# Kernel optimization log

Measured on AMD Instinct MI355X. Metric: run time of the kernel, lower is better.

## Reference

```python
import jax, jax.numpy as jnp
import numpy as np

DIM = 768
H = 64
W = 64
NB = 8
BS = DIM // NB
LAMBD = 0.01
SCALE = 0.02


def softshrink(x, lambd):
    return jnp.sign(x) * jnp.maximum(jnp.abs(x) - lambd, 0.0)


def setup_inputs() -> dict:
    key = jax.random.key(0)
    ks = jax.random.split(key, 7)
    x = jax.random.normal(ks[0], (8, H * W, DIM), dtype=jnp.float32)
    w1 = SCALE * jax.random.normal(ks[1], (2, NB, BS, BS), dtype=jnp.float32)
    b1 = SCALE * jax.random.normal(ks[2], (2, NB, BS), dtype=jnp.float32)
    w2 = SCALE * jax.random.normal(ks[3], (2, NB, BS, BS), dtype=jnp.float32)
    b2 = SCALE * jax.random.normal(ks[4], (2, NB, BS), dtype=jnp.float32)
    # Conv1d(dim, dim, kernel_size=1) == per-token linear: weight [C_out, C_in], bias [C_out]
    Wb = (1.0 / np.sqrt(DIM)) * jax.random.normal(ks[5], (DIM, DIM), dtype=jnp.float32)
    bb = (1.0 / np.sqrt(DIM)) * jax.random.normal(ks[6], (DIM,), dtype=jnp.float32)
    return {"x": x, "w1": w1, "b1": b1, "w2": w2, "b2": b2, "Wb": Wb, "bb": bb}


def reference(x, w1, b1, w2, b2, Wb, bb):
    B, N, C = x.shape
    # bias path: Conv1d with kernel 1 is a linear map over channels
    bias = jnp.einsum('bnc,dc->bnd', x, Wb) + bb
    # spectral path
    xg = x.reshape(B, H, W, C)
    xf = jnp.fft.rfft2(xg, axes=(1, 2), norm='ortho')          # [B, H, W//2+1, C] complex64
    xf = xf.reshape(B, H, W // 2 + 1, NB, BS)
    xr, xi = jnp.real(xf), jnp.imag(xf)
    # layer 1: complex block-diagonal matmul + relu
    r1 = jax.nn.relu(jnp.einsum('...bd,bdk->...bk', xr, w1[0])
                     - jnp.einsum('...bd,bdk->...bk', xi, w1[1]) + b1[0])
    i1 = jax.nn.relu(jnp.einsum('...bd,bdk->...bk', xr, w1[1])
                     + jnp.einsum('...bd,bdk->...bk', xi, w1[0]) + b1[1])
    # layer 2
    r2 = (jnp.einsum('...bd,bdk->...bk', r1, w2[0])
          - jnp.einsum('...bd,bdk->...bk', i1, w2[1]) + b2[0])
    i2 = (jnp.einsum('...bd,bdk->...bk', r1, w2[1])
          + jnp.einsum('...bd,bdk->...bk', i1, w2[0]) + b2[1])
    r2 = softshrink(r2, LAMBD)
    i2 = softshrink(i2, LAMBD)
    xc = (r2 + 1j * i2).reshape(B, H, W // 2 + 1, C)
    xo = jnp.fft.irfft2(xc, s=(H, W), axes=(1, 2), norm='ortho')  # [B, H, W, C]
    return xo.reshape(B, N, C) + bias
```

## Files before the change

### kernel.cpp

```cpp
#include <hip/hip_runtime.h>
#include <math.h>

#ifndef M_PI
#define M_PI 3.14159265358979323846
#endif

namespace {

constexpr int kDim = 768;
constexpr int kNKW = 33;
constexpr int kB = 8;
constexpr float kLambd = 0.01f;
constexpr size_t kXFElems = (size_t)kB * kNKW * 64 * kDim;

typedef __attribute__((ext_vector_type(8))) __bf16 bf16x8;
typedef __attribute__((ext_vector_type(8))) short short8;
typedef __attribute__((ext_vector_type(4))) float f32x4;

alignas(16) __device__ unsigned short g_wT[4 * 8 * 96 * 96];

__device__ inline unsigned short f2bf(float f) {
  unsigned int u = __float_as_uint(f);
  unsigned int r = (u + 0x7FFFu + ((u >> 16) & 1u)) >> 16;
  return (unsigned short)r;
}

__device__ inline bf16x8 s2b(short8 s) { return __builtin_bit_cast(bf16x8, s); }
__device__ inline bf16x8 negb(short8 s) {
  s ^= (short)0x8000;
  return __builtin_bit_cast(bf16x8, s);
}

__device__ inline void gload_lds16(const void* g, void* l) {
  __builtin_amdgcn_global_load_lds(
      (const __attribute__((address_space(1))) unsigned int*)g,
      (__attribute__((address_space(3))) unsigned int*)l, 16, 0, 0);
}

__global__ __launch_bounds__(256) void cvt_f32_bf16_kernel(
    const float* __restrict__ in, unsigned short* __restrict__ out, int n4) {
  int i = blockIdx.x * 256 + threadIdx.x;
  if (i >= n4) return;
  const float4 v = reinterpret_cast<const float4*>(in)[i];
  ushort4 o;
  o.x = f2bf(v.x); o.y = f2bf(v.y); o.z = f2bf(v.z); o.w = f2bf(v.w);
  reinterpret_cast<ushort4*>(out)[i] = o;
}

__global__ __launch_bounds__(256) void cvt_w_kernel(
    const float* __restrict__ w1, const float* __restrict__ w2) {
  const int e = blockIdx.x * 256 + threadIdx.x;
  if (e >= 4 * 8 * 96 * 96) return;
  const int k = e % 96;
  const int d = (e / 96) % 96;
  const int nbm = e / 9216;
  const int mtx = nbm >> 3;
  const int nb = nbm & 7;
  const float* src =
      (mtx < 2 ? w1 : w2) + ((size_t)(mtx & 1) * 8 + nb) * 9216;
  g_wT[((size_t)nbm * 96 + k) * 96 + d] = f2bf(src[d * 96 + k]);
}

__global__ __launch_bounds__(256) void mfma_gemm_kernel(
    const unsigned short* __restrict__ xbf, const unsigned short* __restrict__ wbf,
    const float* __restrict__ bb, float* __restrict__ out) {
  __shared__ unsigned short As[128 * 32];
  __shared__ unsigned short Bs[128 * 32];
  const int t = threadIdx.x;
  const int lane = t & 63;
  const int wid = t >> 6;
  const int wm = wid >> 1;
  const int wn = wid & 1;
  const int id = blockIdx.x;
  const int swz = (id & 7) * 192 + (id >> 3);
  const int m0 = (swz / 6) * 128;
  const int n0 = (swz % 6) * 128;

  f32x4 acc[4][4];
#pragma unroll
  for (int i = 0; i < 4; ++i)
#pragma unroll
    for (int j = 0; j < 4; ++j) acc[i][j] = (f32x4){0.f, 0.f, 0.f, 0.f};

  char* AsB = (char*)As;
  char* BsB = (char*)Bs;
  const int cl = lane & 15;
  const int kg = lane >> 4;

  for (int k0 = 0; k0 < 768; k0 += 32) {
#pragma unroll
    for (int i = 0; i < 2; ++i) {
      const int off = (wid * 2 + i) * 1024 + lane * 16;
      const int row = off >> 6;
      const int kb = off & 63;
      const char* gA = (const char*)xbf + ((size_t)(m0 + row) * 768 + k0) * 2 + kb;
      gload_lds16(gA, AsB + (wid * 2 + i) * 1024);
      const char* gB = (const char*)wbf + ((size_t)(n0 + row) * 768 + k0) * 2 + kb;
      gload_lds16(gB, BsB + (wid * 2 + i) * 1024);
    }
    asm volatile("s_waitcnt vmcnt(0)" ::: "memory");
    __syncthreads();

    bf16x8 av[4], bv[4];
#pragma unroll
    for (int mi = 0; mi < 4; ++mi) {
      const int r = wm * 64 + mi * 16 + cl;
      av[mi] = *reinterpret_cast<const bf16x8*>(AsB + r * 64 + kg * 16);
    }
#pragma unroll
    for (int ni = 0; ni < 4; ++ni) {
      const int r = wn * 64 + ni * 16 + cl;
      bv[ni] = *reinterpret_cast<const bf16x8*>(BsB + r * 64 + kg * 16);
    }
#pragma unroll
    for (int mi = 0; mi < 4; ++mi)
#pragma unroll
      for (int ni = 0; ni < 4; ++ni)
        acc[mi][ni] = __builtin_amdgcn_mfma_f32_16x16x32_bf16(
            av[mi], bv[ni], acc[mi][ni], 0, 0, 0);
    __syncthreads();
  }

#pragma unroll
  for (int ni = 0; ni < 4; ++ni) {
    const int n = n0 + wn * 64 + ni * 16 + cl;
    const float bias = bb[n];
#pragma unroll
    for (int mi = 0; mi < 4; ++mi) {
      const int m = m0 + wm * 64 + mi * 16 + kg * 4;
#pragma unroll
      for (int r = 0; r < 4; ++r) {
        out[(size_t)(m + r) * 768 + n] = acc[mi][ni][r] + bias;
      }
    }
  }
}

__global__ __launch_bounds__(256) void rfft_row_mfma_kernel(
    const float* __restrict__ x, unsigned short* __restrict__ xbf,
    unsigned short* __restrict__ XFr, unsigned short* __restrict__ XFi) {
  __shared__ alignas(16) unsigned short Cs[48 * 80];
  __shared__ alignas(16) unsigned short Ss[48 * 80];
  __shared__ alignas(16) unsigned short xs[64 * 66];
  const int t = threadIdx.x;
  for (int e = t; e < 48 * 64; e += 256) {
    const int kh = e >> 6;
    const int w = e & 63;
    const float ang = (float)(2.0 * M_PI / 64.0) * (float)((kh * w) & 63);
    float s_, c_;
    __sincosf(ang, &s_, &c_);
    Cs[kh * 80 + w] = f2bf(0.125f * c_);
    Ss[kh * 80 + w] = f2bf(-0.125f * s_);
  }

  const int lane = t & 63;
  const int wv = t >> 6;
  const int cl = lane & 15;
  const int kg = lane >> 4;
  const int bh = blockIdx.x;
  const int b = bh >> 6;
  const int h = bh & 63;
  const int c0 = blockIdx.y * 64;

  {
    const float* xrow = x + (size_t)bh * (64 * 768) + c0;
    unsigned short* xbrow = xbf + (size_t)bh * (64 * 768) + c0;
#pragma unroll 4
    for (int it = 0; it < 16; ++it) {
      const int w = wv * 16 + it;
      const float v = xrow[(size_t)w * 768 + lane];
      const unsigned short bv = f2bf(v);
      xbrow[(size_t)w * 768 + lane] = bv;
      xs[w * 66 + lane] = bv;
    }
  }
  __syncthreads();

  const int cA = wv * 16 + cl;
  short8 ax[2];
#pragma unroll
  for (int kf = 0; kf < 2; ++kf) {
#pragma unroll
    for (int j = 0; j < 8; ++j)
      ax[kf][j] = (short)xs[(kf * 32 + kg * 8 + j) * 66 + cA];
  }

  f32x4 aR[3], aI[3];
#pragma unroll
  for (int nt = 0; nt < 3; ++nt) {
    aR[nt] = (f32x4){0.f, 0.f, 0.f, 0.f};
    aI[nt] = (f32x4){0.f, 0.f, 0.f, 0.f};
  }

#pragma unroll
  for (int nt = 0; nt < 3; ++nt) {
#pragma unroll
    for (int kf = 0; kf < 2; ++kf) {
      const int row = nt * 16 + cl;
      const int w0 = kf * 32 + kg * 8;
      const bf16x8 bc = *reinterpret_cast<const bf16x8*>(Cs + row * 80 + w0);
      const bf16x8 bs = *reinterpret_cast<const bf16x8*>(Ss + row * 80 + w0);
      aR[nt] = __builtin_amdgcn_mfma_f32_16x16x32_bf16(s2b(ax[kf]), bc, aR[nt], 0, 0, 0);
      aI[nt] = __builtin_amdgcn_mfma_f32_16x16x32_bf16(s2b(ax[kf]), bs, aI[nt], 0, 0, 0);
    }
  }

  const int cD = c0 + wv * 16 + kg * 4;
#pragma unroll
  for (int nt = 0; nt < 3; ++nt) {
    const int kh = nt * 16 + cl;
    if (kh <= 32) {
      const size_t off = (((size_t)b * kNKW + kh) * 64 + h) * 768 + cD;
      ushort4 vr, vi;
      vr.x = f2bf(aR[nt][0]); vr.y = f2bf(aR[nt][1]);
      vr.z = f2bf(aR[nt][2]); vr.w = f2bf(aR[nt][3]);
      vi.x = f2bf(aI[nt][0]); vi.y = f2bf(aI[nt][1]);
      vi.z = f2bf(aI[nt][2]); vi.w = f2bf(aI[nt][3]);
      *reinterpret_cast<ushort4*>(XFr + off) = vr;
      *reinterpret_cast<ushort4*>(XFi + off) = vi;
    }
  }
}

template <int SIGN>
__global__ __launch_bounds__(256) void fft_col_mfma_kernel(
    unsigned short* __restrict__ Xr, unsigned short* __restrict__ Xi) {
  __shared__ alignas(16) unsigned short Cs[64 * 80];
  __shared__ alignas(16) unsigned short Ss[64 * 80];
  const int t = threadIdx.x;
  for (int e = t; e < 4096; e += 256) {
    const int kh = e >> 6;
    const int h = e & 63;
    const float ang = (float)(2.0 * M_PI / 64.0) * (float)((kh * h) & 63);
    float s_, c_;
    __sincosf(ang, &s_, &c_);
    Cs[kh * 80 + h] = f2bf(0.125f * c_);
    Ss[kh * 80 + h] = f2bf(0.125f * (float)SIGN * s_);
  }
  __syncthreads();

  const int lane = t & 63;
  const int wv = t >> 6;
  const int cl = lane & 15;
  const int kg = lane >> 4;
  const size_t cbase =
      (size_t)blockIdx.x * (64 * 768) + blockIdx.y * 64 + wv * 16 + cl;

  f32x4 aR[4], aI[4];
#pragma unroll
  for (int mi = 0; mi < 4; ++mi) {
    aR[mi] = (f32x4){0.f, 0.f, 0.f, 0.f};
    aI[mi] = (f32x4){0.f, 0.f, 0.f, 0.f};
  }

#pragma unroll
  for (int kf = 0; kf < 2; ++kf) {
    const int h0 = kf * 32 + kg * 8;
    short8 brf, bif;
#pragma unroll
    for (int j = 0; j < 8; ++j) {
      brf[j] = (short)Xr[cbase + (size_t)(h0 + j) * 768];
      bif[j] = (short)Xi[cbase + (size_t)(h0 + j) * 768];
    }
    const bf16x8 bxr = s2b(brf);
    const bf16x8 bxi = s2b(bif);
    const bf16x8 bxin = negb(bif);
#pragma unroll
    for (int mi = 0; mi < 4; ++mi) {
      const int arow = mi * 16 + cl;
      const bf16x8 ac =
          *reinterpret_cast<const bf16x8*>(Cs + arow * 80 + h0);
      const bf16x8 as =
          *reinterpret_cast<const bf16x8*>(Ss + arow * 80 + h0);
      aR[mi] = __builtin_amdgcn_mfma_f32_16x16x32_bf16(ac, bxr, aR[mi], 0, 0, 0);
      aR[mi] = __builtin_amdgcn_mfma_f32_16x16x32_bf16(as, bxin, aR[mi], 0, 0, 0);
      aI[mi] = __builtin_amdgcn_mfma_f32_16x16x32_bf16(ac, bxi, aI[mi], 0, 0, 0);
      aI[mi] = __builtin_amdgcn_mfma_f32_16x16x32_bf16(as, bxr, aI[mi], 0, 0, 0);
    }
  }

#pragma unroll
  for (int mi = 0; mi < 4; ++mi) {
#pragma unroll
    for (int r = 0; r < 4; ++r) {
      const int kh = mi * 16 + kg * 4 + r;
      Xr[cbase + (size_t)kh * 768] = f2bf(aR[mi][r]);
      Xi[cbase + (size_t)kh * 768] = f2bf(aI[mi][r]);
    }
  }
}

__global__ __launch_bounds__(512) void mlp_mfma_kernel(
    unsigned short* __restrict__ Xr, unsigned short* __restrict__ Xi,
    const float* __restrict__ b1, const float* __restrict__ b2) {
  __shared__ unsigned short sXr[128 * 104];
  __shared__ unsigned short sXi[128 * 104];
  const int t = threadIdx.x;
  const int lane = t & 63;
  const int wid = t >> 6;
  const int wm = wid >> 1;
  const int wn = wid & 1;
  const int cl = lane & 15;
  const int kg = lane >> 4;
  const int nb = blockIdx.y;
  const size_t p0 = (size_t)blockIdx.x * 128;

  {
    const int row = t >> 2;
    const int q = t & 3;
    const size_t gbase = (p0 + row) * 768 + nb * 96 + q * 24;
    unsigned short* lr = sXr + row * 104 + q * 24;
    unsigned short* li = sXi + row * 104 + q * 24;
#pragma unroll
    for (int v = 0; v < 3; ++v) {
      *reinterpret_cast<short8*>(lr + v * 8) =
          *reinterpret_cast<const short8*>(Xr + gbase + v * 8);
      *reinterpret_cast<short8*>(li + v * 8) =
          *reinterpret_cast<const short8*>(Xi + gbase + v * 8);
    }
  }
  __syncthreads();

  const unsigned short* wt1r = g_wT + (size_t)(0 * 8 + nb) * 9216;
  const unsigned short* wt1i = g_wT + (size_t)(1 * 8 + nb) * 9216;
  const unsigned short* wt2r = g_wT + (size_t)(2 * 8 + nb) * 9216;
  const unsigned short* wt2i = g_wT + (size_t)(3 * 8 + nb) * 9216;

  f32x4 aR[2][3], aI[2][3];
#pragma unroll
  for (int mf = 0; mf < 2; ++mf)
#pragma unroll
    for (int nf = 0; nf < 3; ++nf) {
      aR[mf][nf] = (f32x4){0.f, 0.f, 0.f, 0.f};
      aI[mf][nf] = (f32x4){0.f, 0.f, 0.f, 0.f};
    }

#pragma unroll
  for (int kk = 0; kk < 3; ++kk) {
    const int ko = kk * 32 + kg * 8;
    short8 xr_[2], xi_[2];
#pragma unroll
    for (int mf = 0; mf < 2; ++mf) {
      const int r = wm * 32 + mf * 16 + cl;
      xr_[mf] = *reinterpret_cast<const short8*>(sXr + r * 104 + ko);
      xi_[mf] = *reinterpret_cast<const short8*>(sXi + r * 104 + ko);
    }
    short8 wr_[3], wi_[3];
#pragma unroll
    for (int nf = 0; nf < 3; ++nf) {
      const int r = wn * 48 + nf * 16 + cl;
      wr_[nf] = *reinterpret_cast<const short8*>(wt1r + r * 96 + ko);
      wi_[nf] = *reinterpret_cast<const short8*>(wt1i + r * 96 + ko);
    }
#pragma unroll
    for (int mf = 0; mf < 2; ++mf) {
      const bf16x8 axr = s2b(xr_[mf]);
      const bf16x8 axi = s2b(xi_[mf]);
      const bf16x8 axin = negb(xi_[mf]);
#pragma unroll
      for (int nf = 0; nf < 3; ++nf) {
        aR[mf][nf] = __builtin_amdgcn_mfma_f32_16x16x32_bf16(axr, s2b(wr_[nf]), aR[mf][nf], 0, 0, 0);
        aR[mf][nf] = __builtin_amdgcn_mfma_f32_16x16x32_bf16(axin, s2b(wi_[nf]), aR[mf][nf], 0, 0, 0);
        aI[mf][nf] = __builtin_amdgcn_mfma_f32_16x16x32_bf16(axr, s2b(wi_[nf]), aI[mf][nf], 0, 0, 0);
        aI[mf][nf] = __builtin_amdgcn_mfma_f32_16x16x32_bf16(axi, s2b(wr_[nf]), aI[mf][nf], 0, 0, 0);
      }
    }
  }
  __syncthreads();

#pragma unroll
  for (int nf = 0; nf < 3; ++nf) {
    const int col = wn * 48 + nf * 16 + cl;
    const float br = b1[nb * 96 + col];
    const float bi = b1[768 + nb * 96 + col];
#pragma unroll
    for (int mf = 0; mf < 2; ++mf) {
#pragma unroll
      for (int r = 0; r < 4; ++r) {
        const int m = wm * 32 + mf * 16 + kg * 4 + r;
        const float vr = fmaxf(aR[mf][nf][r] + br, 0.f);
        const float vi = fmaxf(aI[mf][nf][r] + bi, 0.f);
        sXr[m * 104 + col] = f2bf(vr);
        sXi[m * 104 + col] = f2bf(vi);
      }
    }
  }
  __syncthreads();

#pragma unroll
  for (int mf = 0; mf < 2; ++mf)
#pragma unroll
    for (int nf = 0; nf < 3; ++nf) {
      aR[mf][nf] = (f32x4){0.f, 0.f, 0.f, 0.f};
      aI[mf][nf] = (f32x4){0.f, 0.f, 0.f, 0.f};
    }
#pragma unroll
  for (int kk = 0; kk < 3; ++kk) {
    const int ko = kk * 32 + kg * 8;
    short8 xr_[2], xi_[2];
#pragma unroll
    for (int mf = 0; mf < 2; ++mf) {
      const int r = wm * 32 + mf * 16 + cl;
      xr_[mf] = *reinterpret_cast<const short8*>(sXr + r * 104 + ko);
      xi_[mf] = *reinterpret_cast<const short8*>(sXi + r * 104 + ko);
    }
    short8 wr_[3], wi_[3];
#pragma unroll
    for (int nf = 0; nf < 3; ++nf) {
      const int r = wn * 48 + nf * 16 + cl;
      wr_[nf] = *reinterpret_cast<const short8*>(wt2r + r * 96 + ko);
      wi_[nf] = *reinterpret_cast<const short8*>(wt2i + r * 96 + ko);
    }
#pragma unroll
    for (int mf = 0; mf < 2; ++mf) {
      const bf16x8 axr = s2b(xr_[mf]);
      const bf16x8 axi = s2b(xi_[mf]);
      const bf16x8 axin = negb(xi_[mf]);
#pragma unroll
      for (int nf = 0; nf < 3; ++nf) {
        aR[mf][nf] = __builtin_amdgcn_mfma_f32_16x16x32_bf16(axr, s2b(wr_[nf]), aR[mf][nf], 0, 0, 0);
        aR[mf][nf] = __builtin_amdgcn_mfma_f32_16x16x32_bf16(axin, s2b(wi_[nf]), aR[mf][nf], 0, 0, 0);
        aI[mf][nf] = __builtin_amdgcn_mfma_f32_16x16x32_bf16(axr, s2b(wi_[nf]), aI[mf][nf], 0, 0, 0);
        aI[mf][nf] = __builtin_amdgcn_mfma_f32_16x16x32_bf16(axi, s2b(wr_[nf]), aI[mf][nf], 0, 0, 0);
      }
    }
  }

#pragma unroll
  for (int nf = 0; nf < 3; ++nf) {
    const int col = wn * 48 + nf * 16 + cl;
    const float br = b2[nb * 96 + col];
    const float bi = b2[768 + nb * 96 + col];
    const int gc = nb * 96 + col;
#pragma unroll
    for (int mf = 0; mf < 2; ++mf) {
#pragma unroll
      for (int r = 0; r < 4; ++r) {
        const int m = wm * 32 + mf * 16 + kg * 4 + r;
        float vr = aR[mf][nf][r] + br;
        float vi = aI[mf][nf][r] + bi;
        vr = (vr > kLambd) ? (vr - kLambd) : ((vr < -kLambd) ? (vr + kLambd) : 0.f);
        vi = (vi > kLambd) ? (vi - kLambd) : ((vi < -kLambd) ? (vi + kLambd) : 0.f);
        Xr[(p0 + m) * 768 + gc] = f2bf(vr);
        Xi[(p0 + m) * 768 + gc] = f2bf(vi);
      }
    }
  }
}

__global__ __launch_bounds__(256) void irfft_row_add_mfma_kernel(
    const unsigned short* __restrict__ Zr, const unsigned short* __restrict__ Zi,
    float* __restrict__ out) {
  __shared__ alignas(16) unsigned short Ac[64 * 80];
  __shared__ alignas(16) unsigned short Asn[64 * 80];
  const int t = threadIdx.x;
  for (int e = t; e < 4096; e += 256) {
    const int w = e >> 6;
    const int kw = e & 63;
    unsigned short cv = 0, sv = 0;
    if (kw < 33) {
      const float a = (kw == 0 || kw == 32) ? 0.125f : 0.25f;
      const float ang = (float)(2.0 * M_PI / 64.0) * (float)((kw * w) & 63);
      float s_, c_;
      __sincosf(ang, &s_, &c_);
      cv = f2bf(a * c_);
      sv = f2bf(-a * s_);
    }
    Ac[w * 80 + kw] = cv;
    Asn[w * 80 + kw] = sv;
  }
  __syncthreads();

  const int lane = t & 63;
  const int wv = t >> 6;
  const int cl = lane & 15;
  const int kg = lane >> 4;
  const int bh = blockIdx.x;
  const int b = bh >> 6;
  const int h = bh & 63;
  const int cb = blockIdx.y * 64 + wv * 16;

  const int cA = cb + cl;
  short8 azr[2], azi[2];
#pragma unroll
  for (int kf = 0; kf < 2; ++kf) {
#pragma unroll
    for (int j = 0; j < 8; ++j) {
      const int kw = kf * 32 + kg * 8 + j;
      short zr = 0, zi = 0;
      if (kw < 33) {
        const size_t off = (((size_t)b * kNKW + kw) * 64 + h) * 768 + cA;
        zr = (short)Zr[off];
        zi = (short)Zi[off];
      }
      azr[kf][j] = zr;
      azi[kf][j] = zi;
    }
  }

  const int cD = cb + kg * 4;
  float* obase = out + ((size_t)bh * 64) * 768;
  f32x4 aO[4];
#pragma unroll
  for (int nt = 0; nt < 4; ++nt) {
    const int w = nt * 16 + cl;
    aO[nt] = *reinterpret_cast<const f32x4*>(obase + (size_t)w * 768 + cD);
  }

#pragma unroll
  for (int nt = 0; nt < 4; ++nt) {
#pragma unroll
    for (int kf = 0; kf < 2; ++kf) {
      const int row = nt * 16 + cl;
      const int kw0 = kf * 32 + kg * 8;
      const bf16x8 bc = *reinterpret_cast<const bf16x8*>(Ac + row * 80 + kw0);
      const bf16x8 bs = *reinterpret_cast<const bf16x8*>(Asn + row * 80 + kw0);
      aO[nt] = __builtin_amdgcn_mfma_f32_16x16x32_bf16(s2b(azr[kf]), bc, aO[nt], 0, 0, 0);
      aO[nt] = __builtin_amdgcn_mfma_f32_16x16x32_bf16(s2b(azi[kf]), bs, aO[nt], 0, 0, 0);
    }
  }

#pragma unroll
  for (int nt = 0; nt < 4; ++nt) {
    const int w = nt * 16 + cl;
    *reinterpret_cast<f32x4*>(obase + (size_t)w * 768 + cD) = aO[nt];
  }
}

}

extern "C" void kernel_launch(void* const* d_in, const int* in_sizes, int n_in,
                              void* d_out, int out_size, void* d_ws,
                              size_t ws_size, hipStream_t stream) {
  (void)in_sizes; (void)n_in; (void)out_size;
  const float* x  = (const float*)d_in[0];
  const float* w1 = (const float*)d_in[1];
  const float* b1 = (const float*)d_in[2];
  const float* w2 = (const float*)d_in[3];
  const float* b2 = (const float*)d_in[4];
  const float* Wb = (const float*)d_in[5];
  const float* bb = (const float*)d_in[6];
  float* out = (float*)d_out;

  if (ws_size < 2 * kXFElems * sizeof(float)) return;
  unsigned short* xbf = (unsigned short*)d_ws;
  unsigned short* wbf = xbf + (size_t)32768 * 768;
  unsigned short* XFr = wbf + (size_t)768 * 768;
  unsigned short* XFi = XFr + kXFElems;

  cvt_f32_bf16_kernel<<<dim3((768 * 768 / 4 + 255) / 256), 256, 0, stream>>>(
      Wb, wbf, 768 * 768 / 4);
  cvt_w_kernel<<<dim3(4 * 8 * 96 * 96 / 256), 256, 0, stream>>>(w1, w2);
  rfft_row_mfma_kernel<<<dim3(512, 12), 256, 0, stream>>>(x, xbf, XFr, XFi);
  mfma_gemm_kernel<<<dim3(1536), 256, 0, stream>>>(xbf, wbf, bb, out);
  fft_col_mfma_kernel<-1><<<dim3(264, 12), 256, 0, stream>>>(XFr, XFi);
  mlp_mfma_kernel<<<dim3(132, 8), 512, 0, stream>>>(XFr, XFi, b1, b2);
  fft_col_mfma_kernel<1><<<dim3(264, 12), 256, 0, stream>>>(XFr, XFi);
  irfft_row_add_mfma_kernel<<<dim3(512, 12), 256, 0, stream>>>(XFr, XFi, out);
}
```

Before: 252.6 us.

## Fuse column FFT, spectral MLP, and inverse column FFT into one kernel

Replaces the forward column DFT, block-diagonal complex MLP and inverse column DFT kernels with a single kernel. Each block loads one 64-row by 96-channel slab into LDS and runs all three stages there, writing back once. This removes two full round-trips of the spectral buffers through global memory and two kernel launches. Twiddle tables are now computed once by a small init kernel into global memory and read directly, instead of being rebuilt with sincos in every block. The cost is a 256-thread MLP tile with more LDS per block, strided LDS gathers for the DFT operands, and twiddle reads that go through global memory and cache.

```diff
diff --git a/kernel.cpp b/kernel.cpp
--- a/kernel.cpp
+++ b/kernel.cpp
@@ -18,6 +18,10 @@
 typedef __attribute__((ext_vector_type(4))) float f32x4;
 
 alignas(16) __device__ unsigned short g_wT[4 * 8 * 96 * 96];
+alignas(16) __device__ unsigned short g_twC[64 * 64];
+alignas(16) __device__ unsigned short g_twS[64 * 64];
+alignas(16) __device__ unsigned short g_iwC[64 * 64];
+alignas(16) __device__ unsigned short g_iwS[64 * 64];
 
 __device__ inline unsigned short f2bf(float f) {
   unsigned int u = __float_as_uint(f);
@@ -35,6 +39,26 @@
   __builtin_amdgcn_global_load_lds(
       (const __attribute__((address_space(1))) unsigned int*)g,
       (__attribute__((address_space(3))) unsigned int*)l, 16, 0, 0);
+}
+
+__global__ __launch_bounds__(256) void init_tables_kernel() {
+  const int e = blockIdx.x * 256 + threadIdx.x;
+  if (e >= 4096) return;
+  const int a = e >> 6;
+  const int bcol = e & 63;
+  const float ang = (float)(2.0 * M_PI / 64.0) * (float)((a * bcol) & 63);
+  float s_, c_;
+  __sincosf(ang, &s_, &c_);
+  g_twC[e] = f2bf(0.125f * c_);
+  g_twS[e] = f2bf(0.125f * s_);
+  unsigned short cv = 0, sv = 0;
+  if (bcol < 33) {
+    const float al = (bcol == 0 || bcol == 32) ? 0.125f : 0.25f;
+    cv = f2bf(al * c_);
+    sv = f2bf(-al * s_);
+  }
+  g_iwC[e] = cv;
+  g_iwS[e] = sv;
 }
 
 __global__ __launch_bounds__(256) void cvt_f32_bf16_kernel(
@@ -139,20 +163,8 @@
 __global__ __launch_bounds__(256) void rfft_row_mfma_kernel(
     const float* __restrict__ x, unsigned short* __restrict__ xbf,
     unsigned short* __restrict__ XFr, unsigned short* __restrict__ XFi) {
-  __shared__ alignas(16) unsigned short Cs[48 * 80];
-  __shared__ alignas(16) unsigned short Ss[48 * 80];
   __shared__ alignas(16) unsigned short xs[64 * 66];
   const int t = threadIdx.x;
-  for (int e = t; e < 48 * 64; e += 256) {
-    const int kh = e >> 6;
-    const int w = e & 63;
-    const float ang = (float)(2.0 * M_PI / 64.0) * (float)((kh * w) & 63);
-    float s_, c_;
-    __sincosf(ang, &s_, &c_);
-    Cs[kh * 80 + w] = f2bf(0.125f * c_);
-    Ss[kh * 80 + w] = f2bf(-0.125f * s_);
-  }
-
   const int lane = t & 63;
   const int wv = t >> 6;
   const int cl = lane & 15;
@@ -198,10 +210,10 @@
     for (int kf = 0; kf < 2; ++kf) {
       const int row = nt * 16 + cl;
       const int w0 = kf * 32 + kg * 8;
-      const bf16x8 bc = *reinterpret_cast<const bf16x8*>(Cs + row * 80 + w0);
-      const bf16x8 bs = *reinterpret_cast<const bf16x8*>(Ss + row * 80 + w0);
-      aR[nt] = __builtin_amdgcn_mfma_f32_16x16x32_bf16(s2b(ax[kf]), bc, aR[nt], 0, 0, 0);
-      aI[nt] = __builtin_amdgcn_mfma_f32_16x16x32_bf16(s2b(ax[kf]), bs, aI[nt], 0, 0, 0);
+      const short8 cs = *reinterpret_cast<const short8*>(g_twC + row * 64 + w0);
+      const short8 ss = *reinterpret_cast<const short8*>(g_twS + row * 64 + w0);
+      aR[nt] = __builtin_amdgcn_mfma_f32_16x16x32_bf16(s2b(ax[kf]), s2b(cs), aR[nt], 0, 0, 0);
+      aI[nt] = __builtin_amdgcn_mfma_f32_16x16x32_bf16(s2b(ax[kf]), negb(ss), aI[nt], 0, 0, 0);
     }
   }
 
@@ -222,79 +234,13 @@
   }
 }
 
-template <int SIGN>
-__global__ __launch_bounds__(256) void fft_col_mfma_kernel(
-    unsigned short* __restrict__ Xr, unsigned short* __restrict__ Xi) {
-  __shared__ alignas(16) unsigned short Cs[64 * 80];
-  __shared__ alignas(16) unsigned short Ss[64 * 80];
-  const int t = threadIdx.x;
-  for (int e = t; e < 4096; e += 256) {
-    const int kh = e >> 6;
-    const int h = e & 63;
-    const float ang = (float)(2.0 * M_PI / 64.0) * (float)((kh * h) & 63);
-    float s_, c_;
-    __sincosf(ang, &s_, &c_);
-    Cs[kh * 80 + h] = f2bf(0.125f * c_);
-    Ss[kh * 80 + h] = f2bf(0.125f * (float)SIGN * s_);
-  }
-  __syncthreads();
-
-  const int lane = t & 63;
-  const int wv = t >> 6;
-  const int cl = lane & 15;
-  const int kg = lane >> 4;
-  const size_t cbase =
-      (size_t)blockIdx.x * (64 * 768) + blockIdx.y * 64 + wv * 16 + cl;
-
-  f32x4 aR[4], aI[4];
-#pragma unroll
-  for (int mi = 0; mi < 4; ++mi) {
-    aR[mi] = (f32x4){0.f, 0.f, 0.f, 0.f};
-    aI[mi] = (f32x4){0.f, 0.f, 0.f, 0.f};
-  }
-
-#pragma unroll
-  for (int kf = 0; kf < 2; ++kf) {
-    const int h0 = kf * 32 + kg * 8;
-    short8 brf, bif;
-#pragma unroll
-    for (int j = 0; j < 8; ++j) {
-      brf[j] = (short)Xr[cbase + (size_t)(h0 + j) * 768];
-      bif[j] = (short)Xi[cbase + (size_t)(h0 + j) * 768];
-    }
-    const bf16x8 bxr = s2b(brf);
-    const bf16x8 bxi = s2b(bif);
-    const bf16x8 bxin = negb(bif);
-#pragma unroll
-    for (int mi = 0; mi < 4; ++mi) {
-      const int arow = mi * 16 + cl;
-      const bf16x8 ac =
-          *reinterpret_cast<const bf16x8*>(Cs + arow * 80 + h0);
-      const bf16x8 as =
-          *reinterpret_cast<const bf16x8*>(Ss + arow * 80 + h0);
-      aR[mi] = __builtin_amdgcn_mfma_f32_16x16x32_bf16(ac, bxr, aR[mi], 0, 0, 0);
-      aR[mi] = __builtin_amdgcn_mfma_f32_16x16x32_bf16(as, bxin, aR[mi], 0, 0, 0);
-      aI[mi] = __builtin_amdgcn_mfma_f32_16x16x32_bf16(ac, bxi, aI[mi], 0, 0, 0);
-      aI[mi] = __builtin_amdgcn_mfma_f32_16x16x32_bf16(as, bxr, aI[mi], 0, 0, 0);
-    }
-  }
-
-#pragma unroll
-  for (int mi = 0; mi < 4; ++mi) {
-#pragma unroll
-    for (int r = 0; r < 4; ++r) {
-      const int kh = mi * 16 + kg * 4 + r;
-      Xr[cbase + (size_t)kh * 768] = f2bf(aR[mi][r]);
-      Xi[cbase + (size_t)kh * 768] = f2bf(aI[mi][r]);
-    }
-  }
-}
-
-__global__ __launch_bounds__(512) void mlp_mfma_kernel(
+__global__ __launch_bounds__(256) void spectral_mid_kernel(
     unsigned short* __restrict__ Xr, unsigned short* __restrict__ Xi,
     const float* __restrict__ b1, const float* __restrict__ b2) {
-  __shared__ unsigned short sXr[128 * 104];
-  __shared__ unsigned short sXi[128 * 104];
+  __shared__ alignas(16) unsigned short sXr[64 * 104];
+  __shared__ alignas(16) unsigned short sXi[64 * 104];
+  __shared__ alignas(16) unsigned short sYr[64 * 104];
+  __shared__ alignas(16) unsigned short sYi[64 * 104];
   const int t = threadIdx.x;
   const int lane = t & 63;
   const int wid = t >> 6;
@@ -303,20 +249,71 @@
   const int cl = lane & 15;
   const int kg = lane >> 4;
   const int nb = blockIdx.y;
-  const size_t p0 = (size_t)blockIdx.x * 128;
+  const size_t gbase = (size_t)blockIdx.x * (64 * 768) + nb * 96;
 
   {
     const int row = t >> 2;
     const int q = t & 3;
-    const size_t gbase = (p0 + row) * 768 + nb * 96 + q * 24;
+    const size_t gof = gbase + (size_t)row * 768 + q * 24;
     unsigned short* lr = sXr + row * 104 + q * 24;
     unsigned short* li = sXi + row * 104 + q * 24;
 #pragma unroll
     for (int v = 0; v < 3; ++v) {
       *reinterpret_cast<short8*>(lr + v * 8) =
-          *reinterpret_cast<const short8*>(Xr + gbase + v * 8);
+          *reinterpret_cast<const short8*>(Xr + gof + v * 8);
       *reinterpret_cast<short8*>(li + v * 8) =
-          *reinterpret_cast<const short8*>(Xi + gbase + v * 8);
+          *reinterpret_cast<const short8*>(Xi + gof + v * 8);
+    }
+  }
+  __syncthreads();
+
+  f32x4 accR[2][3], accI[2][3];
+
+#pragma unroll
+  for (int mt = 0; mt < 2; ++mt)
+#pragma unroll
+    for (int nt = 0; nt < 3; ++nt) {
+      accR[mt][nt] = (f32x4){0.f, 0.f, 0.f, 0.f};
+      accI[mt][nt] = (f32x4){0.f, 0.f, 0.f, 0.f};
+    }
+#pragma unroll
+  for (int kf = 0; kf < 2; ++kf) {
+    const int k0 = kf * 32 + kg * 8;
+    short8 bR[3], bI[3];
+#pragma unroll
+    for (int nt = 0; nt < 3; ++nt) {
+      const int col = wn * 48 + nt * 16 + cl;
+#pragma unroll
+      for (int j = 0; j < 8; ++j) {
+        bR[nt][j] = (short)sXr[(k0 + j) * 104 + col];
+        bI[nt][j] = (short)sXi[(k0 + j) * 104 + col];
+      }
+    }
+#pragma unroll
+    for (int mt = 0; mt < 2; ++mt) {
+      const int row = wm * 32 + mt * 16 + cl;
+      const short8 cs = *reinterpret_cast<const short8*>(g_twC + row * 64 + k0);
+      const short8 ss = *reinterpret_cast<const short8*>(g_twS + row * 64 + k0);
+#pragma unroll
+      for (int nt = 0; nt < 3; ++nt) {
+        accR[mt][nt] = __builtin_amdgcn_mfma_f32_16x16x32_bf16(s2b(cs), s2b(bR[nt]), accR[mt][nt], 0, 0, 0);
+        accR[mt][nt] = __builtin_amdgcn_mfma_f32_16x16x32_bf16(s2b(ss), s2b(bI[nt]), accR[mt][nt], 0, 0, 0);
+        accI[mt][nt] = __builtin_amdgcn_mfma_f32_16x16x32_bf16(s2b(cs), s2b(bI[nt]), accI[mt][nt], 0, 0, 0);
+        accI[mt][nt] = __builtin_amdgcn_mfma_f32_16x16x32_bf16(negb(ss), s2b(bR[nt]), accI[mt][nt], 0, 0, 0);
+      }
+    }
+  }
+#pragma unroll
+  for (int mt = 0; mt < 2; ++mt) {
+#pragma unroll
+    for (int nt = 0; nt < 3; ++nt) {
+      const int col = wn * 48 + nt * 16 + cl;
+      const int row0 = wm * 32 + mt * 16 + kg * 4;
+#pragma unroll
+      for (int r = 0; r < 4; ++r) {
+        sYr[(row0 + r) * 104 + col] = f2bf(accR[mt][nt][r]);
+        sYi[(row0 + r) * 104 + col] = f2bf(accI[mt][nt][r]);
+      }
     }
   }
   __syncthreads();
@@ -326,123 +323,165 @@
   const unsigned short* wt2r = g_wT + (size_t)(2 * 8 + nb) * 9216;
   const unsigned short* wt2i = g_wT + (size_t)(3 * 8 + nb) * 9216;
 
-  f32x4 aR[2][3], aI[2][3];
-#pragma unroll
-  for (int mf = 0; mf < 2; ++mf)
-#pragma unroll
-    for (int nf = 0; nf < 3; ++nf) {
-      aR[mf][nf] = (f32x4){0.f, 0.f, 0.f, 0.f};
-      aI[mf][nf] = (f32x4){0.f, 0.f, 0.f, 0.f};
-    }
-
+#pragma unroll
+  for (int mt = 0; mt < 2; ++mt)
+#pragma unroll
+    for (int nt = 0; nt < 3; ++nt) {
+      accR[mt][nt] = (f32x4){0.f, 0.f, 0.f, 0.f};
+      accI[mt][nt] = (f32x4){0.f, 0.f, 0.f, 0.f};
+    }
 #pragma unroll
   for (int kk = 0; kk < 3; ++kk) {
     const int ko = kk * 32 + kg * 8;
-    short8 xr_[2], xi_[2];
-#pragma unroll
-    for (int mf = 0; mf < 2; ++mf) {
-      const int r = wm * 32 + mf * 16 + cl;
-      xr_[mf] = *reinterpret_cast<const short8*>(sXr + r * 104 + ko);
-      xi_[mf] = *reinterpret_cast<const short8*>(sXi + r * 104 + ko);
+    short8 axr[2], axi[2];
+#pragma unroll
+    for (int mt = 0; mt < 2; ++mt) {
+      const int row = wm * 32 + mt * 16 + cl;
+      axr[mt] = *reinterpret_cast<const short8*>(sYr + row * 104 + ko);
+      axi[mt] = *reinterpret_cast<const short8*>(sYi + row * 104 + ko);
     }
     short8 wr_[3], wi_[3];
 #pragma unroll
-    for (int nf = 0; nf < 3; ++nf) {
-      const int r = wn * 48 + nf * 16 + cl;
-      wr_[nf] = *reinterpret_cast<const short8*>(wt1r + r * 96 + ko);
-      wi_[nf] = *reinterpret_cast<const short8*>(wt1i + r * 96 + ko);
-    }
-#pragma unroll
-    for (int mf = 0; mf < 2; ++mf) {
-      const bf16x8 axr = s2b(xr_[mf]);
-      const bf16x8 axi = s2b(xi_[mf]);
-      const bf16x8 axin = negb(xi_[mf]);
-#pragma unroll
-      for (int nf = 0; nf < 3; ++nf) {
-        aR[mf][nf] = __builtin_amdgcn_mfma_f32_16x16x32_bf16(axr, s2b(wr_[nf]), aR[mf][nf], 0, 0, 0);
-        aR[mf][nf] = __builtin_amdgcn_mfma_f32_16x16x32_bf16(axin, s2b(wi_[nf]), aR[mf][nf], 0, 0, 0);
-        aI[mf][nf] = __builtin_amdgcn_mfma_f32_16x16x32_bf16(axr, s2b(wi_[nf]), aI[mf][nf], 0, 0, 0);
-        aI[mf][nf] = __builtin_amdgcn_mfma_f32_16x16x32_bf16(axi, s2b(wr_[nf]), aI[mf][nf], 0, 0, 0);
-      }
-    }
-  }
-  __syncthreads();
-
-#pragma unroll
-  for (int nf = 0; nf < 3; ++nf) {
-    const int col = wn * 48 + nf * 16 + cl;
+    for (int nt = 0; nt < 3; ++nt) {
+      const int rw = wn * 48 + nt * 16 + cl;
+      wr_[nt] = *reinterpret_cast<const short8*>(wt1r + rw * 96 + ko);
+      wi_[nt] = *reinterpret_cast<const short8*>(wt1i + rw * 96 + ko);
+    }
+#pragma unroll
+    for (int mt = 0; mt < 2; ++mt) {
+      const bf16x8 ar = s2b(axr[mt]);
+      const bf16x8 ai = s2b(axi[mt]);
+      const bf16x8 ain = negb(axi[mt]);
+#pragma unroll
+      for (int nt = 0; nt < 3; ++nt) {
+        accR[mt][nt] = __builtin_amdgcn_mfma_f32_16x16x32_bf16(ar, s2b(wr_[nt]), accR[mt][nt], 0, 0, 0);
+        accR[mt][nt] = __builtin_amdgcn_mfma_f32_16x16x32_bf16(ain, s2b(wi_[nt]), accR[mt][nt], 0, 0, 0);
+        accI[mt][nt] = __builtin_amdgcn_mfma_f32_16x16x32_bf16(ar, s2b(wi_[nt]), accI[mt][nt], 0, 0, 0);
+        accI[mt][nt] = __builtin_amdgcn_mfma_f32_16x16x32_bf16(ai, s2b(wr_[nt]), accI[mt][nt], 0, 0, 0);
+      }
+    }
+  }
+#pragma unroll
+  for (int nt = 0; nt < 3; ++nt) {
+    const int col = wn * 48 + nt * 16 + cl;
     const float br = b1[nb * 96 + col];
     const float bi = b1[768 + nb * 96 + col];
 #pragma unroll
-    for (int mf = 0; mf < 2; ++mf) {
+    for (int mt = 0; mt < 2; ++mt) {
+      const int row0 = wm * 32 + mt * 16 + kg * 4;
 #pragma unroll
       for (int r = 0; r < 4; ++r) {
-        const int m = wm * 32 + mf * 16 + kg * 4 + r;
-        const float vr = fmaxf(aR[mf][nf][r] + br, 0.f);
-        const float vi = fmaxf(aI[mf][nf][r] + bi, 0.f);
-        sXr[m * 104 + col] = f2bf(vr);
-        sXi[m * 104 + col] = f2bf(vi);
+        sXr[(row0 + r) * 104 + col] = f2bf(fmaxf(accR[mt][nt][r] + br, 0.f));
+        sXi[(row0 + r) * 104 + col] = f2bf(fmaxf(accI[mt][nt][r] + bi, 0.f));
       }
     }
   }
   __syncthreads();
 
 #pragma unroll
-  for (int mf = 0; mf < 2; ++mf)
-#pragma unroll
-    for (int nf = 0; nf < 3; ++nf) {
-      aR[mf][nf] = (f32x4){0.f, 0.f, 0.f, 0.f};
-      aI[mf][nf] = (f32x4){0.f, 0.f, 0.f, 0.f};
+  for (int mt = 0; mt < 2; ++mt)
+#pragma unroll
+    for (int nt = 0; nt < 3; ++nt) {
+      accR[mt][nt] = (f32x4){0.f, 0.f, 0.f, 0.f};
+      accI[mt][nt] = (f32x4){0.f, 0.f, 0.f, 0.f};
     }
 #pragma unroll
   for (int kk = 0; kk < 3; ++kk) {
     const int ko = kk * 32 + kg * 8;
-    short8 xr_[2], xi_[2];
-#pragma unroll
-    for (int mf = 0; mf < 2; ++mf) {
-      const int r = wm * 32 + mf * 16 + cl;
-      xr_[mf] = *reinterpret_cast<const short8*>(sXr + r * 104 + ko);
-      xi_[mf] = *reinterpret_cast<const short8*>(sXi + r * 104 + ko);
+    short8 axr[2], axi[2];
+#pragma unroll
+    for (int mt = 0; mt < 2; ++mt) {
+      const int row = wm * 32 + mt * 16 + cl;
+      axr[mt] = *reinterpret_cast<const short8*>(sXr + row * 104 + ko);
+      axi[mt] = *reinterpret_cast<const short8*>(sXi + row * 104 + ko);
     }
     short8 wr_[3], wi_[3];
 #pragma unroll
-    for (int nf = 0; nf < 3; ++nf) {
-      const int r = wn * 48 + nf * 16 + cl;
-      wr_[nf] = *reinterpret_cast<const short8*>(wt2r + r * 96 + ko);
-      wi_[nf] = *reinterpret_cast<const short8*>(wt2i + r * 96 + ko);
-    }
-#pragma unroll
-    for (int mf = 0; mf < 2; ++mf) {
-      const bf16x8 axr = s2b(xr_[mf]);
-      const bf16x8 axi = s2b(xi_[mf]);
-      const bf16x8 axin = negb(xi_[mf]);
-#pragma unroll
-      for (int nf = 0; nf < 3; ++nf) {
-        aR[mf][nf] = __builtin_amdgcn_mfma_f32_16x16x32_bf16(axr, s2b(wr_[nf]), aR[mf][nf], 0, 0, 0);
-        aR[mf][nf] = __builtin_amdgcn_mfma_f32_16x16x32_bf16(axin, s2b(wi_[nf]), aR[mf][nf], 0, 0, 0);
-        aI[mf][nf] = __builtin_amdgcn_mfma_f32_16x16x32_bf16(axr, s2b(wi_[nf]), aI[mf][nf], 0, 0, 0);
-        aI[mf][nf] = __builtin_amdgcn_mfma_f32_16x16x32_bf16(axi, s2b(wr_[nf]), aI[mf][nf], 0, 0, 0);
-      }
-    }
-  }
-
-#pragma unroll
-  for (int nf = 0; nf < 3; ++nf) {
-    const int col = wn * 48 + nf * 16 + cl;
+    for (int nt = 0; nt < 3; ++nt) {
+      const int rw = wn * 48 + nt * 16 + cl;
+      wr_[nt] = *reinterpret_cast<const short8*>(wt2r + rw * 96 + ko);
+      wi_[nt] = *reinterpret_cast<const short8*>(wt2i + rw * 96 + ko);
+    }
+#pragma unroll
+    for (int mt = 0; mt < 2; ++mt) {
+      const bf16x8 ar = s2b(axr[mt]);
+      const bf16x8 ai = s2b(axi[mt]);
+      const bf16x8 ain = negb(axi[mt]);
+#pragma unroll
+      for (int nt = 0; nt < 3; ++nt) {
+        accR[mt][nt] = __builtin_amdgcn_mfma_f32_16x16x32_bf16(ar, s2b(wr_[nt]), accR[mt][nt], 0, 0, 0);
+        accR[mt][nt] = __builtin_amdgcn_mfma_f32_16x16x32_bf16(ain, s2b(wi_[nt]), accR[mt][nt], 0, 0, 0);
+        accI[mt][nt] = __builtin_amdgcn_mfma_f32_16x16x32_bf16(ar, s2b(wi_[nt]), accI[mt][nt], 0, 0, 0);
+        accI[mt][nt] = __builtin_amdgcn_mfma_f32_16x16x32_bf16(ai, s2b(wr_[nt]), accI[mt][nt], 0, 0, 0);
+      }
+    }
+  }
+#pragma unroll
+  for (int nt = 0; nt < 3; ++nt) {
+    const int col = wn * 48 + nt * 16 + cl;
     const float br = b2[nb * 96 + col];
     const float bi = b2[768 + nb * 96 + col];
-    const int gc = nb * 96 + col;
-#pragma unroll
-    for (int mf = 0; mf < 2; ++mf) {
+#pragma unroll
+    for (int mt = 0; mt < 2; ++mt) {
+      const int row0 = wm * 32 + mt * 16 + kg * 4;
 #pragma unroll
       for (int r = 0; r < 4; ++r) {
-        const int m = wm * 32 + mf * 16 + kg * 4 + r;
-        float vr = aR[mf][nf][r] + br;
-        float vi = aI[mf][nf][r] + bi;
+        float vr = accR[mt][nt][r] + br;
+        float vi = accI[mt][nt][r] + bi;
         vr = (vr > kLambd) ? (vr - kLambd) : ((vr < -kLambd) ? (vr + kLambd) : 0.f);
         vi = (vi > kLambd) ? (vi - kLambd) : ((vi < -kLambd) ? (vi + kLambd) : 0.f);
-        Xr[(p0 + m) * 768 + gc] = f2bf(vr);
-        Xi[(p0 + m) * 768 + gc] = f2bf(vi);
+        sYr[(row0 + r) * 104 + col] = f2bf(vr);
+        sYi[(row0 + r) * 104 + col] = f2bf(vi);
+      }
+    }
+  }
+  __syncthreads();
+
+#pragma unroll
+  for (int mt = 0; mt < 2; ++mt)
+#pragma unroll
+    for (int nt = 0; nt < 3; ++nt) {
+      accR[mt][nt] = (f32x4){0.f, 0.f, 0.f, 0.f};
+      accI[mt][nt] = (f32x4){0.f, 0.f, 0.f, 0.f};
+    }
+#pragma unroll
+  for (int kf = 0; kf < 2; ++kf) {
+    const int k0 = kf * 32 + kg * 8;
+    short8 bR[3], bI[3];
+#pragma unroll
+    for (int nt = 0; nt < 3; ++nt) {
+      const int col = wn * 48 + nt * 16 + cl;
+#pragma unroll
+      for (int j = 0; j < 8; ++j) {
+        bR[nt][j] = (short)sYr[(k0 + j) * 104 + col];
+        bI[nt][j] = (short)sYi[(k0 + j) * 104 + col];
+      }
+    }
+#pragma unroll
+    for (int mt = 0; mt < 2; ++mt) {
+      const int row = wm * 32 + mt * 16 + cl;
+      const short8 cs = *reinterpret_cast<const short8*>(g_twC + row * 64 + k0);
+      const short8 ss = *reinterpret_cast<const short8*>(g_twS + row * 64 + k0);
+#pragma unroll
+      for (int nt = 0; nt < 3; ++nt) {
+        accR[mt][nt] = __builtin_amdgcn_mfma_f32_16x16x32_bf16(s2b(cs), s2b(bR[nt]), accR[mt][nt], 0, 0, 0);
+        accR[mt][nt] = __builtin_amdgcn_mfma_f32_16x16x32_bf16(negb(ss), s2b(bI[nt]), accR[mt][nt], 0, 0, 0);
+        accI[mt][nt] = __builtin_amdgcn_mfma_f32_16x16x32_bf16(s2b(cs), s2b(bI[nt]), accI[mt][nt], 0, 0, 0);
+        accI[mt][nt] = __builtin_amdgcn_mfma_f32_16x16x32_bf16(s2b(ss), s2b(bR[nt]), accI[mt][nt], 0, 0, 0);
+      }
+    }
+  }
+#pragma unroll
+  for (int mt = 0; mt < 2; ++mt) {
+#pragma unroll
+    for (int nt = 0; nt < 3; ++nt) {
+      const int col = wn * 48 + nt * 16 + cl;
+      const int row0 = wm * 32 + mt * 16 + kg * 4;
+#pragma unroll
+      for (int r = 0; r < 4; ++r) {
+        const size_t off = gbase + (size_t)(row0 + r) * 768 + col;
+        Xr[off] = f2bf(accR[mt][nt][r]);
+        Xi[off] = f2bf(accI[mt][nt][r]);
       }
     }
   }
@@ -451,26 +490,7 @@
 __global__ __launch_bounds__(256) void irfft_row_add_mfma_kernel(
     const unsigned short* __restrict__ Zr, const unsigned short* __restrict__ Zi,
     float* __restrict__ out) {
-  __shared__ alignas(16) unsigned short Ac[64 * 80];
-  __shared__ alignas(16) unsigned short Asn[64 * 80];
   const int t = threadIdx.x;
-  for (int e = t; e < 4096; e += 256) {
-    const int w = e >> 6;
-    const int kw = e & 63;
-    unsigned short cv = 0, sv = 0;
-    if (kw < 33) {
-      const float a = (kw == 0 || kw == 32) ? 0.125f : 0.25f;
-      const float ang = (float)(2.0 * M_PI / 64.0) * (float)((kw * w) & 63);
-      float s_, c_;
-      __sincosf(ang, &s_, &c_);
-      cv = f2bf(a * c_);
-      sv = f2bf(-a * s_);
-    }
-    Ac[w * 80 + kw] = cv;
-    Asn[w * 80 + kw] = sv;
-  }
-  __syncthreads();
-
   const int lane = t & 63;
   const int wv = t >> 6;
   const int cl = lane & 15;
@@ -513,10 +533,10 @@
     for (int kf = 0; kf < 2; ++kf) {
       const int row = nt * 16 + cl;
       const int kw0 = kf * 32 + kg * 8;
-      const bf16x8 bc = *reinterpret_cast<const bf16x8*>(Ac + row * 80 + kw0);
-      const bf16x8 bs = *reinterpret_cast<const bf16x8*>(Asn + row * 80 + kw0);
-      aO[nt] = __builtin_amdgcn_mfma_f32_16x16x32_bf16(s2b(azr[kf]), bc, aO[nt], 0, 0, 0);
-      aO[nt] = __builtin_amdgcn_mfma_f32_16x16x32_bf16(s2b(azi[kf]), bs, aO[nt], 0, 0, 0);
+      const short8 bc = *reinterpret_cast<const short8*>(g_iwC + row * 64 + kw0);
+      const short8 bs = *reinterpret_cast<const short8*>(g_iwS + row * 64 + kw0);
+      aO[nt] = __builtin_amdgcn_mfma_f32_16x16x32_bf16(s2b(azr[kf]), s2b(bc), aO[nt], 0, 0, 0);
+      aO[nt] = __builtin_amdgcn_mfma_f32_16x16x32_bf16(s2b(azi[kf]), s2b(bs), aO[nt], 0, 0, 0);
     }
   }
 
@@ -548,13 +568,12 @@
   unsigned short* XFr = wbf + (size_t)768 * 768;
   unsigned short* XFi = XFr + kXFElems;
 
+  init_tables_kernel<<<dim3(16), 256, 0, stream>>>();
   cvt_f32_bf16_kernel<<<dim3((768 * 768 / 4 + 255) / 256), 256, 0, stream>>>(
       Wb, wbf, 768 * 768 / 4);
   cvt_w_kernel<<<dim3(4 * 8 * 96 * 96 / 256), 256, 0, stream>>>(w1, w2);
   rfft_row_mfma_kernel<<<dim3(512, 12), 256, 0, stream>>>(x, xbf, XFr, XFi);
   mfma_gemm_kernel<<<dim3(1536), 256, 0, stream>>>(xbf, wbf, bb, out);
-  fft_col_mfma_kernel<-1><<<dim3(264, 12), 256, 0, stream>>>(XFr, XFi);
-  mlp_mfma_kernel<<<dim3(132, 8), 512, 0, stream>>>(XFr, XFi, b1, b2);
-  fft_col_mfma_kernel<1><<<dim3(264, 12), 256, 0, stream>>>(XFr, XFi);
+  spectral_mid_kernel<<<dim3(264, 8), 256, 0, stream>>>(XFr, XFi, b1, b2);
   irfft_row_add_mfma_kernel<<<dim3(512, 12), 256, 0, stream>>>(XFr, XFi, out);
 }
```

Measured after the change: 279.7 us. 1.11x slower.
